# Performance work log

Measured on AMD Instinct MI355X. Metric: run time of the kernel, lower is better.

The kernel has to match this reference:

```python
import jax, jax.numpy as jnp
import numpy as np
from math import sqrt

N = 50000      # n_nodes
M = 800000     # n_edges (avg degree 16)
D = 256        # d_Embedding
H = 8          # heads
DK = 32        # per-head key/query dim
DV = 32        # per-head value dim


def setup_inputs() -> dict:
    key = jax.random.key(0)
    ks = jax.random.split(key, 10)
    s = 0.02
    x = jax.random.normal(ks[0], (N, D), dtype=jnp.float32)
    edge_index = jax.random.randint(ks[1], (2, M), 0, N, dtype=jnp.int32)
    # projection weights stored pre-reshaped to (D, H, dhead); equivalent to nn.Linear(D, H*dhead)
    Wk = jax.random.normal(ks[2], (D, H, DK), dtype=jnp.float32) * s
    bk = jax.random.normal(ks[3], (H, DK), dtype=jnp.float32) * s
    Wq = jax.random.normal(ks[4], (D, H, DK), dtype=jnp.float32) * s
    bq = jax.random.normal(ks[5], (H, DK), dtype=jnp.float32) * s
    Wv = jax.random.normal(ks[6], (D, H, DV), dtype=jnp.float32) * s
    bv = jax.random.normal(ks[7], (H, DV), dtype=jnp.float32) * s
    Wagg = jax.random.normal(ks[8], (H * DV, D), dtype=jnp.float32) * s
    bagg = jnp.zeros((D,), dtype=jnp.float32)
    Wff = jax.random.normal(ks[9], (D, D), dtype=jnp.float32) * s
    bff = jnp.zeros((D,), dtype=jnp.float32)
    return {"x": x, "edge_index": edge_index, "Wk": Wk, "bk": bk, "Wq": Wq,
            "bq": bq, "Wv": Wv, "bv": bv, "Wagg": Wagg, "bagg": bagg,
            "Wff": Wff, "bff": bff}


def reference(x, edge_index, Wk, bk, Wq, bq, Wv, bv, Wagg, bagg, Wff, bff):
    recv = edge_index[0]
    send = edge_index[1]
    # per-head projections: (N, H, d)
    K = jnp.einsum('nd,dhk->nhk', x, Wk) + bk
    Q = jnp.einsum('nd,dhk->nhk', x, Wq) + bq
    V = jnp.einsum('nd,dhv->nhv', x, Wv) + bv
    # edge-wise attention logits: (M, H)
    qk = jnp.sum(Q[recv] * K[send], axis=-1)
    # faithful to original: rescale by 3/global_max, then exp
    att = jnp.exp(qk * 3.0 / jnp.max(qk))
    # segment-softmax normalization over edges sharing a receiver
    sums = jax.ops.segment_sum(att, recv, num_segments=N)  # (N, H)
    att = att / sums[recv] / sqrt(DK)
    # weighted scatter-add of sender values: (N, H, DV)
    msg = att[..., None] * V[send]
    out = jax.ops.segment_sum(msg, recv, num_segments=N)
    out = jax.nn.relu(out).reshape(N, H * DV)
    out = jax.nn.relu(out @ Wagg + bagg)
    out = jax.nn.relu(out @ Wff + bff)
    return x + out
```

## Files before the change

kernel.cpp:

```cpp
#include <hip/hip_runtime.h>

#define N_NODES 50000
#define M_EDGES 800000
#define RP 50048

typedef __bf16 bf16x8 __attribute__((ext_vector_type(8)));
typedef __bf16 bf16x4 __attribute__((ext_vector_type(4)));
typedef float  f32x4  __attribute__((ext_vector_type(4)));

static __device__ __forceinline__ unsigned enc_ord(float f) {
    unsigned b = __float_as_uint(f);
    return (b & 0x80000000u) ? ~b : (b | 0x80000000u);
}
static __device__ __forceinline__ float dec_ord(unsigned u) {
    unsigned b = (u & 0x80000000u) ? (u ^ 0x80000000u) : ~u;
    return __uint_as_float(b);
}
static __device__ __forceinline__ float bflo(unsigned u) { return __uint_as_float(u << 16); }
static __device__ __forceinline__ float bfhi(unsigned u) { return __uint_as_float(u & 0xffff0000u); }
static __device__ __forceinline__ unsigned short bfbits(__bf16 b) {
    unsigned short u; __builtin_memcpy(&u, &b, 2); return u;
}

static __device__ __forceinline__ size_t PE(int m, int k) {
    return (size_t)(m >> 7) * 32768 + (size_t)(k >> 5) * 4096 +
           (size_t)((k >> 3) & 3) * 1024 + (size_t)(m & 127) * 8 + (k & 7);
}

static __device__ __forceinline__ void gload16(const void* g, void* l) {
    __builtin_amdgcn_global_load_lds(
        (const __attribute__((address_space(1))) void*)g,
        (__attribute__((address_space(3))) void*)l, 16, 0, 0);
}

static __device__ __forceinline__ void stage_panel(
    const char* a0, const char* a1, const char* b0, const char* b1,
    char* lds0, int buf, int t, int tid) {
    size_t so = (size_t)t * 8192 + (size_t)tid * 16;
    size_t lo = (size_t)buf * 32768 + (size_t)tid * 16;
    gload16(a0 + so, lds0 + lo);
    gload16(a0 + so + 4096, lds0 + lo + 4096);
    gload16(a1 + so, lds0 + 8192 + lo);
    gload16(a1 + so + 4096, lds0 + 8192 + lo + 4096);
    gload16(b0 + so, lds0 + 16384 + lo);
    gload16(b0 + so + 4096, lds0 + 16384 + lo + 4096);
    gload16(b1 + so, lds0 + 24576 + lo);
    gload16(b1 + so + 4096, lds0 + 24576 + lo + 4096);
}

__global__ __launch_bounds__(256) void prep_kernel(
    const float* __restrict__ Wk, const float* __restrict__ Wq,
    const float* __restrict__ Wv, const float* __restrict__ Wagg,
    const float* __restrict__ Wff,
    const float* __restrict__ bk, const float* __restrict__ bq,
    const float* __restrict__ bv,
    const float* __restrict__ X,
    __bf16* __restrict__ WHq, __bf16* __restrict__ WLq,
    __bf16* __restrict__ WaH, __bf16* __restrict__ WaL,
    __bf16* __restrict__ WfH, __bf16* __restrict__ WfL,
    float* __restrict__ bqkv, __bf16* __restrict__ xh, __bf16* __restrict__ xl,
    int* __restrict__ counts, int* __restrict__ cursor, unsigned* __restrict__ gmax) {
    int gid = blockIdx.x * 256 + threadIdx.x;
    int stride = gridDim.x * 256;
    for (int i = gid; i < 65536; i += stride) {
        int n = i >> 8, k = i & 255;
        size_t src = (size_t)k * 256 + n;
        float v; __bf16 h;
        v = Wk[src];   h = (__bf16)v; WHq[PE(n, k)] = h;
                       WLq[PE(n, k)] = (__bf16)(v - (float)h);
        v = Wq[src];   h = (__bf16)v; WHq[PE(n + 256, k)] = h;
                       WLq[PE(n + 256, k)] = (__bf16)(v - (float)h);
        v = Wv[src];   h = (__bf16)v; WHq[PE(n + 512, k)] = h;
                       WLq[PE(n + 512, k)] = (__bf16)(v - (float)h);
        v = Wagg[src]; h = (__bf16)v; WaH[PE(n, k)] = h;
                       WaL[PE(n, k)] = (__bf16)(v - (float)h);
        v = Wff[src];  h = (__bf16)v; WfH[PE(n, k)] = h;
                       WfL[PE(n, k)] = (__bf16)(v - (float)h);
    }
    const size_t nx = (size_t)N_NODES * 256 / 4;
    for (size_t i = gid; i < nx; i += stride) {
        float4 v = *(const float4*)(X + i * 4);
        int n = (int)(i >> 6), k0 = (int)((i * 4) & 255);
        bf16x4 hh, ll;
        hh[0] = (__bf16)v.x; ll[0] = (__bf16)(v.x - (float)hh[0]);
        hh[1] = (__bf16)v.y; ll[1] = (__bf16)(v.y - (float)hh[1]);
        hh[2] = (__bf16)v.z; ll[2] = (__bf16)(v.z - (float)hh[2]);
        hh[3] = (__bf16)v.w; ll[3] = (__bf16)(v.w - (float)hh[3]);
        size_t idx = PE(n, k0);
        *(bf16x4*)(xh + idx) = hh;
        *(bf16x4*)(xl + idx) = ll;
    }
    for (int i = gid; i < 768; i += stride)
        bqkv[i] = (i < 256) ? bk[i] : ((i < 512) ? bq[i - 256] : bv[i - 512]);
    for (int i = gid; i < N_NODES; i += stride) { counts[i] = 0; cursor[i] = 0; }
    if (gid == 0) *gmax = 0u;
}

__global__ __launch_bounds__(256) void gemm_qkv(
    const __bf16* __restrict__ AhP, const __bf16* __restrict__ AlP,
    const __bf16* __restrict__ BhP, const __bf16* __restrict__ BlP,
    const float* __restrict__ bqkv,
    __bf16* __restrict__ Kb, float* __restrict__ Qo, __bf16* __restrict__ Vb) {
    __shared__ __attribute__((aligned(16))) __bf16 sm[2][4][4][128][8];

    const int NB = 2346, q = NB / 8, r = NB % 8;
    int bid = blockIdx.x;
    int xcd = bid & 7, i0 = bid >> 3;
    int logical = (xcd < r ? xcd * (q + 1) : r * (q + 1) + (xcd - r) * q) + i0;
    int by = logical % 6;
    int bx = logical / 6;
    int row0 = bx * 128;
    int n0   = by * 128;

    int tid  = threadIdx.x;
    int lane = tid & 63, wave = tid >> 6;
    int wm = (wave >> 1) * 64, wn = (wave & 1) * 64;

    f32x4 acc[4][4];
    #pragma unroll
    for (int i = 0; i < 4; i++)
        #pragma unroll
        for (int j = 0; j < 4; j++) acc[i][j] = (f32x4)(0.f);

    const char* a0 = (const char*)AhP + (size_t)bx * 65536;
    const char* a1 = (const char*)AlP + (size_t)bx * 65536;
    const char* b0 = (const char*)BhP + (size_t)by * 65536;
    const char* b1 = (const char*)BlP + (size_t)by * 65536;
    char* lds0 = (char*)&sm[0][0][0][0][0];

    stage_panel(a0, a1, b0, b1, lds0, 0, 0, tid);
    __syncthreads();

    int h = lane >> 4;
    int m_base = wm + (lane & 15);
    int n_base = wn + (lane & 15);

    for (int t = 0; t < 8; t++) {
        int cur = t & 1;
        if (t < 7) stage_panel(a0, a1, b0, b1, lds0, cur ^ 1, t + 1, tid);
        bf16x8 ahf[4], alf[4], bhf[4], blf[4];
        #pragma unroll
        for (int mt = 0; mt < 4; mt++) {
            ahf[mt] = *(const bf16x8*)&sm[cur][0][h][m_base + mt * 16][0];
            alf[mt] = *(const bf16x8*)&sm[cur][1][h][m_base + mt * 16][0];
        }
        #pragma unroll
        for (int nt = 0; nt < 4; nt++) {
            bhf[nt] = *(const bf16x8*)&sm[cur][2][h][n_base + nt * 16][0];
            blf[nt] = *(const bf16x8*)&sm[cur][3][h][n_base + nt * 16][0];
        }
        #pragma unroll
        for (int mt = 0; mt < 4; mt++)
            #pragma unroll
            for (int nt = 0; nt < 4; nt++) {
                acc[mt][nt] = __builtin_amdgcn_mfma_f32_16x16x32_bf16(ahf[mt], bhf[nt], acc[mt][nt], 0, 0, 0);
                acc[mt][nt] = __builtin_amdgcn_mfma_f32_16x16x32_bf16(alf[mt], bhf[nt], acc[mt][nt], 0, 0, 0);
                acc[mt][nt] = __builtin_amdgcn_mfma_f32_16x16x32_bf16(ahf[mt], blf[nt], acc[mt][nt], 0, 0, 0);
            }
        __syncthreads();
    }

    #pragma unroll
    for (int mt = 0; mt < 4; mt++) {
        #pragma unroll
        for (int nt = 0; nt < 4; nt++) {
            int cg = n0 + wn + nt * 16 + (lane & 15);
            #pragma unroll
            for (int rr = 0; rr < 4; rr++) {
                int row = row0 + wm + mt * 16 + (lane >> 4) * 4 + rr;
                if (row < N_NODES) {
                    float v = acc[mt][nt][rr] + bqkv[cg];
                    if (cg < 256)      Kb[(size_t)row * 256 + cg] = (__bf16)v;
                    else if (cg < 512) Qo[(size_t)row * 256 + (cg - 256)] = v;
                    else               Vb[(size_t)row * 256 + (cg - 512)] = (__bf16)v;
                }
            }
        }
    }
}

__global__ void hist_kernel(const int* __restrict__ recv, int* __restrict__ counts) {
    int t = blockIdx.x * 256 + threadIdx.x;
    if (t < M_EDGES) atomicAdd(&counts[recv[t]], 1);
}

__global__ void scan_kernel(const int* __restrict__ counts, int* __restrict__ offsets) {
    __shared__ int part[256];
    int t = threadIdx.x;
    const int per = (N_NODES + 255) / 256;
    int start = t * per;
    int end = min(start + per, N_NODES);
    int s = 0;
    for (int i = start; i < end; i++) s += counts[i];
    part[t] = s;
    __syncthreads();
    if (t == 0) {
        int acc = 0;
        for (int i = 0; i < 256; i++) { int v = part[i]; part[i] = acc; acc += v; }
    }
    __syncthreads();
    int acc = part[t];
    for (int i = start; i < end; i++) { offsets[i] = acc; acc += counts[i]; }
    if (end == N_NODES && start < N_NODES) offsets[N_NODES] = acc;
}

__global__ void fill_kernel(const int* __restrict__ recv, const int* __restrict__ send,
                            const int* __restrict__ offsets,
                            int* __restrict__ cursor, int* __restrict__ ssorted,
                            int* __restrict__ rsorted) {
    int t = blockIdx.x * 256 + threadIdx.x;
    if (t < M_EDGES) {
        int r = recv[t];
        int pos = offsets[r] + atomicAdd(&cursor[r], 1);
        ssorted[pos] = send[t];
        rsorted[pos] = r;
    }
}

__global__ __launch_bounds__(256) void qk_csr_kernel(
    const int* __restrict__ ssorted, const int* __restrict__ rsorted,
    const float* __restrict__ Q, const unsigned short* __restrict__ Kb,
    float* __restrict__ qks, unsigned* __restrict__ gmax) {
    int wave_id = (blockIdx.x * 256 + threadIdx.x) >> 6;
    int lane = threadIdx.x & 63;
    int e_slot = lane >> 5;
    int sl = lane & 31;
    const int nwaves = (gridDim.x * 256) >> 6;
    const int npairs = M_EDGES / 2;
    float wmax = -INFINITY;
    for (int pp = wave_id; pp < npairs; pp += 4 * nwaves) {
        int ep[4]; bool valid[4];
        #pragma unroll
        for (int u = 0; u < 4; u++) {
            int p = pp + u * nwaves;
            valid[u] = p < npairs;
            ep[u] = (valid[u] ? p : pp) * 2 + e_slot;
        }
        int si[4], ri[4];
        #pragma unroll
        for (int u = 0; u < 4; u++) { si[u] = ssorted[ep[u]]; ri[u] = rsorted[ep[u]]; }
        uint4 kv[4]; float4 qa[4], qb[4];
        #pragma unroll
        for (int u = 0; u < 4; u++) {
            kv[u] = *(const uint4*)(Kb + (size_t)si[u] * 256 + sl * 8);
            qa[u] = *(const float4*)(Q + (size_t)ri[u] * 256 + sl * 8);
            qb[u] = *(const float4*)(Q + (size_t)ri[u] * 256 + sl * 8 + 4);
        }
        #pragma unroll
        for (int u = 0; u < 4; u++) {
            float d = qa[u].x * bflo(kv[u].x) + qa[u].y * bfhi(kv[u].x)
                    + qa[u].z * bflo(kv[u].y) + qa[u].w * bfhi(kv[u].y)
                    + qb[u].x * bflo(kv[u].z) + qb[u].y * bfhi(kv[u].z)
                    + qb[u].z * bflo(kv[u].w) + qb[u].w * bfhi(kv[u].w);
            d += __shfl_xor(d, 1);
            d += __shfl_xor(d, 2);
            wmax = fmaxf(wmax, d);
            if ((sl & 3) == 0 && valid[u])
                qks[(size_t)ep[u] * 8 + (sl >> 2)] = d;
        }
    }
    wmax = fmaxf(wmax, __shfl_xor(wmax, 1));
    wmax = fmaxf(wmax, __shfl_xor(wmax, 2));
    wmax = fmaxf(wmax, __shfl_xor(wmax, 4));
    wmax = fmaxf(wmax, __shfl_xor(wmax, 8));
    wmax = fmaxf(wmax, __shfl_xor(wmax, 16));
    wmax = fmaxf(wmax, __shfl_xor(wmax, 32));
    if (lane == 0 && wmax > -INFINITY) atomicMax(gmax, enc_ord(wmax));
}

__global__ __launch_bounds__(256) void node_agg_kernel(
    const int* __restrict__ offsets, const int* __restrict__ ssorted,
    const float* __restrict__ qks, const unsigned short* __restrict__ Vb,
    const unsigned* __restrict__ gmax,
    __bf16* __restrict__ msgH, __bf16* __restrict__ msgL) {
    int wave_id = (blockIdx.x * 256 + threadIdx.x) >> 6;
    int lane = threadIdx.x & 63;
    int h = lane >> 3;
    const int nwaves = (gridDim.x * 256) >> 6;
    const int per = (N_NODES + nwaves - 1) / nwaves;
    int n0 = wave_id * per;
    int nend = min(n0 + per, N_NODES);
    float scale = 3.0f / dec_ord(*gmax);
    for (int n = n0; n < nend; n++) {
        int off = offsets[n];
        int deg = offsets[n + 1] - off;
        float sum = 0.f, a0 = 0.f, a1 = 0.f, a2 = 0.f, a3 = 0.f;
        for (int b = 0; b < deg; b += 64) {
            int bn = min(64, deg - b);
            int idxb = ssorted[off + b + min(lane, bn - 1)];
            #define VROW(i) (*(const uint2*)(Vb + \
                (size_t)__shfl(idxb, min((i), bn - 1)) * 256 + lane * 4))
            #define QKL(i) qks[(size_t)(off + b + min((i), bn - 1)) * 8 + h]
            uint2 v0 = VROW(0);
            uint2 v1 = VROW(1);
            float q0 = QKL(0);
            float q1 = QKL(1);
            for (int i = 0; i < bn; i++) {
                uint2 vc = v0; v0 = v1; v1 = VROW(i + 2);
                float qc = q0; q0 = q1; q1 = QKL(i + 2);
                float a = __expf(qc * scale);
                sum += a;
                a0 += a * bflo(vc.x); a1 += a * bfhi(vc.x);
                a2 += a * bflo(vc.y); a3 += a * bfhi(vc.y);
            }
            #undef VROW
            #undef QKL
        }
        float inv = (deg > 0) ? 1.0f / (sum * 5.65685424949238f) : 0.f;
        float r0 = fmaxf(a0 * inv, 0.f), r1 = fmaxf(a1 * inv, 0.f);
        float r2 = fmaxf(a2 * inv, 0.f), r3 = fmaxf(a3 * inv, 0.f);
        bf16x4 hv, lv;
        hv[0] = (__bf16)r0; lv[0] = (__bf16)(r0 - (float)hv[0]);
        hv[1] = (__bf16)r1; lv[1] = (__bf16)(r1 - (float)hv[1]);
        hv[2] = (__bf16)r2; lv[2] = (__bf16)(r2 - (float)hv[2]);
        hv[3] = (__bf16)r3; lv[3] = (__bf16)(r3 - (float)hv[3]);
        size_t idx = PE(n, lane * 4);
        *(bf16x4*)(msgH + idx) = hv;
        *(bf16x4*)(msgL + idx) = lv;
    }
}

__global__ __launch_bounds__(256) void mlp_fused(
    const __bf16* __restrict__ msgHP, const __bf16* __restrict__ msgLP,
    const __bf16* __restrict__ WaHP, const __bf16* __restrict__ WaLP,
    const __bf16* __restrict__ WfHP, const __bf16* __restrict__ WfLP,
    const float* __restrict__ bagg, const float* __restrict__ bff,
    const float* __restrict__ x, float* __restrict__ out) {
    __shared__ __attribute__((aligned(16))) __bf16 sm[2][4][4][128][8];

    int row0 = blockIdx.x * 128;
    int bxp  = blockIdx.x;
    int tid  = threadIdx.x;
    int lane = tid & 63, wave = tid >> 6;
    int wm = (wave >> 1) * 64, wn = (wave & 1) * 64;
    char* lds0 = (char*)&sm[0][0][0][0][0];
    int h = lane >> 4;
    int m_base = wm + (lane & 15);
    int n_base = wn + (lane & 15);

    f32x4 acc1[2][4][4];
    #pragma unroll
    for (int nh = 0; nh < 2; nh++)
        #pragma unroll
        for (int i = 0; i < 4; i++)
            #pragma unroll
            for (int j = 0; j < 4; j++) acc1[nh][i][j] = (f32x4)(0.f);

    const char* a0 = (const char*)msgHP + (size_t)bxp * 65536;
    const char* a1 = (const char*)msgLP + (size_t)bxp * 65536;

    #pragma unroll
    for (int nh = 0; nh < 2; nh++) {
        const char* b0 = (const char*)WaHP + (size_t)nh * 65536;
        const char* b1 = (const char*)WaLP + (size_t)nh * 65536;
        stage_panel(a0, a1, b0, b1, lds0, 0, 0, tid);
        __syncthreads();
        for (int t = 0; t < 8; t++) {
            int cur = t & 1;
            if (t < 7) stage_panel(a0, a1, b0, b1, lds0, cur ^ 1, t + 1, tid);
            bf16x8 ahf[4], alf[4], bhf[4], blf[4];
            #pragma unroll
            for (int mt = 0; mt < 4; mt++) {
                ahf[mt] = *(const bf16x8*)&sm[cur][0][h][m_base + mt * 16][0];
                alf[mt] = *(const bf16x8*)&sm[cur][1][h][m_base + mt * 16][0];
            }
            #pragma unroll
            for (int nt = 0; nt < 4; nt++) {
                bhf[nt] = *(const bf16x8*)&sm[cur][2][h][n_base + nt * 16][0];
                blf[nt] = *(const bf16x8*)&sm[cur][3][h][n_base + nt * 16][0];
            }
            #pragma unroll
            for (int mt = 0; mt < 4; mt++)
                #pragma unroll
                for (int nt = 0; nt < 4; nt++) {
                    acc1[nh][mt][nt] = __builtin_amdgcn_mfma_f32_16x16x32_bf16(ahf[mt], bhf[nt], acc1[nh][mt][nt], 0, 0, 0);
                    acc1[nh][mt][nt] = __builtin_amdgcn_mfma_f32_16x16x32_bf16(alf[mt], bhf[nt], acc1[nh][mt][nt], 0, 0, 0);
                    acc1[nh][mt][nt] = __builtin_amdgcn_mfma_f32_16x16x32_bf16(ahf[mt], blf[nt], acc1[nh][mt][nt], 0, 0, 0);
                }
            __syncthreads();
        }
    }

    unsigned hidp[2][4][4][4];
    #pragma unroll
    for (int nh = 0; nh < 2; nh++)
        #pragma unroll
        for (int mt = 0; mt < 4; mt++)
            #pragma unroll
            for (int nt = 0; nt < 4; nt++)
                #pragma unroll
                for (int rr = 0; rr < 4; rr++) {
                    int col = nh * 128 + wn + nt * 16 + (lane & 15);
                    float v = acc1[nh][mt][nt][rr] + bagg[col];
                    v = fmaxf(v, 0.f);
                    __bf16 hh = (__bf16)v;
                    __bf16 hl = (__bf16)(v - (float)hh);
                    hidp[nh][mt][nt][rr] =
                        (unsigned)bfbits(hh) | ((unsigned)bfbits(hl) << 16);
                }

    unsigned short* chunkw = (unsigned short*)lds0;
    const __bf16*   chunkb = (const __bf16*)lds0;
    char*           b2c    = lds0 + 16384;
    const __bf16*   b2b    = (const __bf16*)(lds0 + 16384);

    for (int oh = 0; oh < 2; oh++) {
        const char* f0 = (const char*)WfHP + (size_t)oh * 65536;
        const char* f1 = (const char*)WfLP + (size_t)oh * 65536;
        f32x4 acc2[4][4];
        #pragma unroll
        for (int i = 0; i < 4; i++)
            #pragma unroll
            for (int j = 0; j < 4; j++) acc2[i][j] = (f32x4)(0.f);

        #pragma unroll
        for (int s = 0; s < 8; s++) {
            __syncthreads();
            int nh = s >> 2, sq = s & 3;
            if (wn == ((sq >= 2) ? 64 : 0)) {
                int nt0 = (sq & 1) * 2;
                #pragma unroll
                for (int mt = 0; mt < 4; mt++)
                    #pragma unroll
                    for (int j = 0; j < 2; j++) {
                        int nt = nt0 + j;
                        int kc = (wn + nt * 16 + (lane & 15)) - 32 * sq;
                        int ks = kc >> 3, e = kc & 7;
                        #pragma unroll
                        for (int rr = 0; rr < 4; rr++) {
                            int row = wm + mt * 16 + (lane >> 4) * 4 + rr;
                            unsigned u = hidp[nh][mt][nt][rr];
                            chunkw[(size_t)ks * 1024 + row * 8 + e] =
                                (unsigned short)(u & 0xffffu);
                            chunkw[(size_t)(4 + ks) * 1024 + row * 8 + e] =
                                (unsigned short)(u >> 16);
                        }
                    }
            }
            {
                size_t so = (size_t)s * 8192 + (size_t)tid * 16;
                size_t lo = (size_t)tid * 16;
                gload16(f0 + so, b2c + lo);
                gload16(f0 + so + 4096, b2c + lo + 4096);
                gload16(f1 + so, b2c + 8192 + lo);
                gload16(f1 + so + 4096, b2c + 8192 + lo + 4096);
            }
            __syncthreads();
            bf16x8 a2h[4], a2l[4], b2h[4], b2l[4];
            #pragma unroll
            for (int mt = 0; mt < 4; mt++) {
                a2h[mt] = *(const bf16x8*)&chunkb[(size_t)h * 1024 + (m_base + mt * 16) * 8];
                a2l[mt] = *(const bf16x8*)&chunkb[(size_t)(4 + h) * 1024 + (m_base + mt * 16) * 8];
            }
            #pragma unroll
            for (int nt = 0; nt < 4; nt++) {
                b2h[nt] = *(const bf16x8*)&b2b[(size_t)h * 1024 + (n_base + nt * 16) * 8];
                b2l[nt] = *(const bf16x8*)&b2b[(size_t)(4 + h) * 1024 + (n_base + nt * 16) * 8];
            }
            #pragma unroll
            for (int mt = 0; mt < 4; mt++)
                #pragma unroll
                for (int nt = 0; nt < 4; nt++) {
                    acc2[mt][nt] = __builtin_amdgcn_mfma_f32_16x16x32_bf16(a2h[mt], b2h[nt], acc2[mt][nt], 0, 0, 0);
                    acc2[mt][nt] = __builtin_amdgcn_mfma_f32_16x16x32_bf16(a2l[mt], b2h[nt], acc2[mt][nt], 0, 0, 0);
                    acc2[mt][nt] = __builtin_amdgcn_mfma_f32_16x16x32_bf16(a2h[mt], b2l[nt], acc2[mt][nt], 0, 0, 0);
                }
        }
        #pragma unroll
        for (int mt = 0; mt < 4; mt++)
            #pragma unroll
            for (int nt = 0; nt < 4; nt++) {
                int oc = oh * 128 + wn + nt * 16 + (lane & 15);
                #pragma unroll
                for (int rr = 0; rr < 4; rr++) {
                    int row = row0 + wm + mt * 16 + (lane >> 4) * 4 + rr;
                    if (row < N_NODES) {
                        float v = acc2[mt][nt][rr] + bff[oc];
                        v = fmaxf(v, 0.f);
                        size_t idx = (size_t)row * 256 + oc;
                        out[idx] = v + x[idx];
                    }
                }
            }
    }
}

extern "C" void kernel_launch(void* const* d_in, const int* in_sizes, int n_in,
                              void* d_out, int out_size, void* d_ws, size_t ws_size,
                              hipStream_t stream) {
    const float* x    = (const float*)d_in[0];
    const int*   edge = (const int*)d_in[1];
    const int*   recv = edge;
    const int*   send = edge + M_EDGES;
    const float* Wk   = (const float*)d_in[2];
    const float* bk   = (const float*)d_in[3];
    const float* Wq   = (const float*)d_in[4];
    const float* bq   = (const float*)d_in[5];
    const float* Wv   = (const float*)d_in[6];
    const float* bv   = (const float*)d_in[7];
    const float* Wagg = (const float*)d_in[8];
    const float* bagg = (const float*)d_in[9];
    const float* Wff  = (const float*)d_in[10];
    const float* bff  = (const float*)d_in[11];
    float* out = (float*)d_out;

    float*  Qbuf  = (float*)d_ws;
    float*  reg2  = Qbuf + (size_t)RP * 256;
    float*  qks   = reg2 + (size_t)RP * 256;
    __bf16* Kbf   = (__bf16*)(qks + (size_t)M_EDGES * 8);
    __bf16* Vbf   = Kbf + (size_t)RP * 256;
    int* counts   = (int*)(Vbf + (size_t)RP * 256);
    int* cursor   = counts + N_NODES;
    int* offsets  = cursor + N_NODES;
    int* ssorted  = offsets + N_NODES + 1;
    unsigned* gmax = (unsigned*)(ssorted + M_EDGES);
    __bf16* wt    = (__bf16*)(gmax + 1);
    __bf16* WHq = wt;
    __bf16* WLq = wt + 3 * 65536;
    __bf16* WaH = wt + 6 * 65536;  __bf16* WaL = wt + 7 * 65536;
    __bf16* WfH = wt + 8 * 65536;  __bf16* WfL = wt + 9 * 65536;
    float* bqkv = (float*)(wt + 10 * 65536);
    __bf16* xh   = (__bf16*)reg2;
    __bf16* xl   = xh + (size_t)RP * 256;
    int*    rsorted = (int*)reg2;
    __bf16* msgH = (__bf16*)reg2;
    __bf16* msgL = msgH + (size_t)RP * 256;

    dim3 blk(256);
    dim3 edge_grid((M_EDGES + 255) / 256);

    hipLaunchKernelGGL(prep_kernel, dim3(2048), blk, 0, stream,
                       Wk, Wq, Wv, Wagg, Wff, bk, bq, bv, x,
                       WHq, WLq, WaH, WaL, WfH, WfL, bqkv, xh, xl,
                       counts, cursor, gmax);
    hipLaunchKernelGGL(gemm_qkv, dim3(2346), blk, 0, stream,
                       xh, xl, WHq, WLq, bqkv, Kbf, Qbuf, Vbf);
    hipLaunchKernelGGL(hist_kernel, edge_grid, blk, 0, stream, recv, counts);
    hipLaunchKernelGGL(scan_kernel, dim3(1), blk, 0, stream, counts, offsets);
    hipLaunchKernelGGL(fill_kernel, edge_grid, blk, 0, stream, recv, send, offsets,
                       cursor, ssorted, rsorted);
    hipLaunchKernelGGL(qk_csr_kernel, dim3(1024), blk, 0, stream,
                       ssorted, rsorted, Qbuf, (const unsigned short*)Kbf, qks, gmax);
    hipLaunchKernelGGL(node_agg_kernel, dim3(2048), blk, 0, stream,
                       offsets, ssorted, qks, (const unsigned short*)Vbf, gmax,
                       msgH, msgL);
    hipLaunchKernelGGL(mlp_fused, dim3((N_NODES + 127) / 128), blk, 0, stream,
                       msgH, msgL, WaH, WaL, WfH, WfL, bagg, bff, x, out);
}
```

Measured before the change: 834.1 us.

## Stage activations in LDS once and read weight fragments directly from global memory

The fused MLP kernel now loads each block's message tile into LDS in two halves, used across both output halves, instead of re-staging activations alongside weights per panel. Wagg and Wff fragments are read straight from global memory, which should hit L2 or cache since all blocks share them, so LDS weight staging and many barriers go away. The second GEMM writes all four hidden sub-chunks per K-half before computing, which cuts synchronization count. The cost is global-load latency on the MFMA critical path without double buffering, and higher register pressure from the full unroll.

New measurement: 825.5 us. About the same (-1.0%).

```diff
diff --git a/kernel.cpp b/kernel.cpp
--- a/kernel.cpp
+++ b/kernel.cpp
@@ -326,18 +326,20 @@
     const __bf16* __restrict__ WfHP, const __bf16* __restrict__ WfLP,
     const float* __restrict__ bagg, const float* __restrict__ bff,
     const float* __restrict__ x, float* __restrict__ out) {
-    __shared__ __attribute__((aligned(16))) __bf16 sm[2][4][4][128][8];
+    __shared__ __attribute__((aligned(16))) __bf16 sm[32768];
 
     int row0 = blockIdx.x * 128;
-    int bxp  = blockIdx.x;
     int tid  = threadIdx.x;
     int lane = tid & 63, wave = tid >> 6;
     int wm = (wave >> 1) * 64, wn = (wave & 1) * 64;
-    char* lds0 = (char*)&sm[0][0][0][0][0];
+    char* lds0 = (char*)sm;
     int h = lane >> 4;
     int m_base = wm + (lane & 15);
     int n_base = wn + (lane & 15);
 
+    const char* a0 = (const char*)msgHP + (size_t)blockIdx.x * 65536;
+    const char* a1 = (const char*)msgLP + (size_t)blockIdx.x * 65536;
+
     f32x4 acc1[2][4][4];
     #pragma unroll
     for (int nh = 0; nh < 2; nh++)
@@ -346,37 +348,60 @@
             #pragma unroll
             for (int j = 0; j < 4; j++) acc1[nh][i][j] = (f32x4)(0.f);
 
-    const char* a0 = (const char*)msgHP + (size_t)bxp * 65536;
-    const char* a1 = (const char*)msgLP + (size_t)bxp * 65536;
-
-    #pragma unroll
-    for (int nh = 0; nh < 2; nh++) {
-        const char* b0 = (const char*)WaHP + (size_t)nh * 65536;
-        const char* b1 = (const char*)WaLP + (size_t)nh * 65536;
-        stage_panel(a0, a1, b0, b1, lds0, 0, 0, tid);
-        __syncthreads();
-        for (int t = 0; t < 8; t++) {
-            int cur = t & 1;
-            if (t < 7) stage_panel(a0, a1, b0, b1, lds0, cur ^ 1, t + 1, tid);
-            bf16x8 ahf[4], alf[4], bhf[4], blf[4];
-            #pragma unroll
-            for (int mt = 0; mt < 4; mt++) {
-                ahf[mt] = *(const bf16x8*)&sm[cur][0][h][m_base + mt * 16][0];
-                alf[mt] = *(const bf16x8*)&sm[cur][1][h][m_base + mt * 16][0];
-            }
-            #pragma unroll
-            for (int nt = 0; nt < 4; nt++) {
-                bhf[nt] = *(const bf16x8*)&sm[cur][2][h][n_base + nt * 16][0];
-                blf[nt] = *(const bf16x8*)&sm[cur][3][h][n_base + nt * 16][0];
-            }
-            #pragma unroll
-            for (int mt = 0; mt < 4; mt++)
+    #pragma unroll
+    for (int tl = 0; tl < 4; tl++) {
+        size_t so = (size_t)tl * 8192 + (size_t)tid * 16;
+        gload16(a0 + so, lds0 + so);
+        gload16(a0 + so + 4096, lds0 + so + 4096);
+        gload16(a1 + so, lds0 + 32768 + so);
+        gload16(a1 + so + 4096, lds0 + 32768 + so + 4096);
+    }
+    __syncthreads();
+
+    #pragma unroll
+    for (int hf = 0; hf < 2; hf++) {
+        #pragma unroll
+        for (int nh = 0; nh < 2; nh++) {
+            const __bf16* wb0 = WaHP + (size_t)nh * 32768;
+            const __bf16* wb1 = WaLP + (size_t)nh * 32768;
+            #pragma unroll
+            for (int tl = 0; tl < 4; tl++) {
+                int t = hf * 4 + tl;
+                const __bf16* lA = (const __bf16*)lds0;
+                bf16x8 ahf[4], alf[4], bhf[4], blf[4];
+                #pragma unroll
+                for (int mt = 0; mt < 4; mt++) {
+                    size_t ai = (size_t)tl * 4096 + (size_t)h * 1024 + (size_t)(m_base + mt * 16) * 8;
+                    ahf[mt] = *(const bf16x8*)&lA[ai];
+                    alf[mt] = *(const bf16x8*)&lA[16384 + ai];
+                }
                 #pragma unroll
                 for (int nt = 0; nt < 4; nt++) {
-                    acc1[nh][mt][nt] = __builtin_amdgcn_mfma_f32_16x16x32_bf16(ahf[mt], bhf[nt], acc1[nh][mt][nt], 0, 0, 0);
-                    acc1[nh][mt][nt] = __builtin_amdgcn_mfma_f32_16x16x32_bf16(alf[mt], bhf[nt], acc1[nh][mt][nt], 0, 0, 0);
-                    acc1[nh][mt][nt] = __builtin_amdgcn_mfma_f32_16x16x32_bf16(ahf[mt], blf[nt], acc1[nh][mt][nt], 0, 0, 0);
-                }
+                    size_t bi = (size_t)t * 4096 + (size_t)h * 1024 + (size_t)(n_base + nt * 16) * 8;
+                    bhf[nt] = *(const bf16x8*)(wb0 + bi);
+                    blf[nt] = *(const bf16x8*)(wb1 + bi);
+                }
+                #pragma unroll
+                for (int mt = 0; mt < 4; mt++)
+                    #pragma unroll
+                    for (int nt = 0; nt < 4; nt++) {
+                        acc1[nh][mt][nt] = __builtin_amdgcn_mfma_f32_16x16x32_bf16(ahf[mt], bhf[nt], acc1[nh][mt][nt], 0, 0, 0);
+                        acc1[nh][mt][nt] = __builtin_amdgcn_mfma_f32_16x16x32_bf16(alf[mt], bhf[nt], acc1[nh][mt][nt], 0, 0, 0);
+                        acc1[nh][mt][nt] = __builtin_amdgcn_mfma_f32_16x16x32_bf16(ahf[mt], blf[nt], acc1[nh][mt][nt], 0, 0, 0);
+                    }
+            }
+        }
+        if (hf == 0) {
+            __syncthreads();
+            #pragma unroll
+            for (int tl = 0; tl < 4; tl++) {
+                size_t so = (size_t)(4 + tl) * 8192 + (size_t)tid * 16;
+                size_t lo = (size_t)tl * 8192 + (size_t)tid * 16;
+                gload16(a0 + so, lds0 + lo);
+                gload16(a0 + so + 4096, lds0 + lo + 4096);
+                gload16(a1 + so, lds0 + 32768 + lo);
+                gload16(a1 + so + 4096, lds0 + 32768 + lo + 4096);
+            }
             __syncthreads();
         }
     }
@@ -399,14 +424,13 @@
                         (unsigned)bfbits(hh) | ((unsigned)bfbits(hl) << 16);
                 }
 
-    unsigned short* chunkw = (unsigned short*)lds0;
-    const __bf16*   chunkb = (const __bf16*)lds0;
-    char*           b2c    = lds0 + 16384;
-    const __bf16*   b2b    = (const __bf16*)(lds0 + 16384);
-
+    unsigned short* w16 = (unsigned short*)lds0;
+    const __bf16*   lB  = (const __bf16*)lds0;
+
+    #pragma unroll
     for (int oh = 0; oh < 2; oh++) {
-        const char* f0 = (const char*)WfHP + (size_t)oh * 65536;
-        const char* f1 = (const char*)WfLP + (size_t)oh * 65536;
+        const __bf16* f0 = WfHP + (size_t)oh * 32768;
+        const __bf16* f1 = WfLP + (size_t)oh * 32768;
         f32x4 acc2[4][4];
         #pragma unroll
         for (int i = 0; i < 4; i++)
@@ -414,57 +438,57 @@
             for (int j = 0; j < 4; j++) acc2[i][j] = (f32x4)(0.f);
 
         #pragma unroll
-        for (int s = 0; s < 8; s++) {
+        for (int kh = 0; kh < 2; kh++) {
             __syncthreads();
-            int nh = s >> 2, sq = s & 3;
-            if (wn == ((sq >= 2) ? 64 : 0)) {
-                int nt0 = (sq & 1) * 2;
+            #pragma unroll
+            for (int sl = 0; sl < 4; sl++) {
+                if (wn == ((sl >= 2) ? 64 : 0)) {
+                    int nt0 = (sl & 1) * 2;
+                    #pragma unroll
+                    for (int mt = 0; mt < 4; mt++)
+                        #pragma unroll
+                        for (int j = 0; j < 2; j++) {
+                            int nt = nt0 + j;
+                            int kc = (wn + nt * 16 + (lane & 15)) - 32 * sl;
+                            int ks = kc >> 3, e = kc & 7;
+                            #pragma unroll
+                            for (int rr = 0; rr < 4; rr++) {
+                                int row = wm + mt * 16 + (lane >> 4) * 4 + rr;
+                                unsigned u = hidp[kh][mt][nt][rr];
+                                w16[(size_t)sl * 4096 + ks * 1024 + row * 8 + e] =
+                                    (unsigned short)(u & 0xffffu);
+                                w16[16384 + (size_t)sl * 4096 + ks * 1024 + row * 8 + e] =
+                                    (unsigned short)(u >> 16);
+                            }
+                        }
+                }
+            }
+            __syncthreads();
+            #pragma unroll
+            for (int tl = 0; tl < 4; tl++) {
+                int t = kh * 4 + tl;
+                bf16x8 a2h[4], a2l[4], b2h[4], b2l[4];
+                #pragma unroll
+                for (int mt = 0; mt < 4; mt++) {
+                    size_t ai = (size_t)tl * 4096 + (size_t)h * 1024 + (size_t)(m_base + mt * 16) * 8;
+                    a2h[mt] = *(const bf16x8*)&lB[ai];
+                    a2l[mt] = *(const bf16x8*)&lB[16384 + ai];
+                }
+                #pragma unroll
+                for (int nt = 0; nt < 4; nt++) {
+                    size_t bi = (size_t)t * 4096 + (size_t)h * 1024 + (size_t)(n_base + nt * 16) * 8;
+                    b2h[nt] = *(const bf16x8*)(f0 + bi);
+                    b2l[nt] = *(const bf16x8*)(f1 + bi);
+                }
                 #pragma unroll
                 for (int mt = 0; mt < 4; mt++)
                     #pragma unroll
-                    for (int j = 0; j < 2; j++) {
-                        int nt = nt0 + j;
-                        int kc = (wn + nt * 16 + (lane & 15)) - 32 * sq;
-                        int ks = kc >> 3, e = kc & 7;
-                        #pragma unroll
-                        for (int rr = 0; rr < 4; rr++) {
-                            int row = wm + mt * 16 + (lane >> 4) * 4 + rr;
-                            unsigned u = hidp[nh][mt][nt][rr];
-                            chunkw[(size_t)ks * 1024 + row * 8 + e] =
-                                (unsigned short)(u & 0xffffu);
-                            chunkw[(size_t)(4 + ks) * 1024 + row * 8 + e] =
-                                (unsigned short)(u >> 16);
-                        }
+                    for (int nt = 0; nt < 4; nt++) {
+                        acc2[mt][nt] = __builtin_amdgcn_mfma_f32_16x16x32_bf16(a2h[mt], b2h[nt], acc2[mt][nt], 0, 0, 0);
+                        acc2[mt][nt] = __builtin_amdgcn_mfma_f32_16x16x32_bf16(a2l[mt], b2h[nt], acc2[mt][nt], 0, 0, 0);
+                        acc2[mt][nt] = __builtin_amdgcn_mfma_f32_16x16x32_bf16(a2h[mt], b2l[nt], acc2[mt][nt], 0, 0, 0);
                     }
             }
-            {
-                size_t so = (size_t)s * 8192 + (size_t)tid * 16;
-                size_t lo = (size_t)tid * 16;
-                gload16(f0 + so, b2c + lo);
-                gload16(f0 + so + 4096, b2c + lo + 4096);
-                gload16(f1 + so, b2c + 8192 + lo);
-                gload16(f1 + so + 4096, b2c + 8192 + lo + 4096);
-            }
-            __syncthreads();
-            bf16x8 a2h[4], a2l[4], b2h[4], b2l[4];
-            #pragma unroll
-            for (int mt = 0; mt < 4; mt++) {
-                a2h[mt] = *(const bf16x8*)&chunkb[(size_t)h * 1024 + (m_base + mt * 16) * 8];
-                a2l[mt] = *(const bf16x8*)&chunkb[(size_t)(4 + h) * 1024 + (m_base + mt * 16) * 8];
-            }
-            #pragma unroll
-            for (int nt = 0; nt < 4; nt++) {
-                b2h[nt] = *(const bf16x8*)&b2b[(size_t)h * 1024 + (n_base + nt * 16) * 8];
-                b2l[nt] = *(const bf16x8*)&b2b[(size_t)(4 + h) * 1024 + (n_base + nt * 16) * 8];
-            }
-            #pragma unroll
-            for (int mt = 0; mt < 4; mt++)
-                #pragma unroll
-                for (int nt = 0; nt < 4; nt++) {
-                    acc2[mt][nt] = __builtin_amdgcn_mfma_f32_16x16x32_bf16(a2h[mt], b2h[nt], acc2[mt][nt], 0, 0, 0);
-                    acc2[mt][nt] = __builtin_amdgcn_mfma_f32_16x16x32_bf16(a2l[mt], b2h[nt], acc2[mt][nt], 0, 0, 0);
-                    acc2[mt][nt] = __builtin_amdgcn_mfma_f32_16x16x32_bf16(a2h[mt], b2l[nt], acc2[mt][nt], 0, 0, 0);
-                }
         }
         #pragma unroll
         for (int mt = 0; mt < 4; mt++)
```

## Restructure fused MLP to 64-row tiles with weights read directly from global

Applied to the files above, without the earlier changes.

The fused two-layer MLP kernel now processes 64 rows per block instead of 128, doubling the grid. Each wave owns 64 output columns across all rows. Only the activation panel is staged in shared memory, while the weight fragments for both GEMMs are loaded straight from global memory (and so from cache) instead of being staged through LDS. The aim is to cut LDS use and synchronisation, raise occupancy, and keep the hidden layer in-block with fewer exchanges. The cost is repeated global weight reads per wave and less A-tile reuse per block.

Measured after the change: 769.5 us. 1.08x faster.

```diff
diff --git a/kernel.cpp b/kernel.cpp
--- a/kernel.cpp
+++ b/kernel.cpp
@@ -326,136 +326,142 @@
     const __bf16* __restrict__ WfHP, const __bf16* __restrict__ WfLP,
     const float* __restrict__ bagg, const float* __restrict__ bff,
     const float* __restrict__ x, float* __restrict__ out) {
-    __shared__ __attribute__((aligned(16))) __bf16 sm[2][4][4][128][8];
-
-    int row0 = blockIdx.x * 128;
-    int bxp  = blockIdx.x;
+    __shared__ __attribute__((aligned(16))) __bf16 sm[16384];
+
+    int row0 = blockIdx.x * 64;
+    int p    = blockIdx.x >> 1;
+    int sb   = blockIdx.x & 1;
     int tid  = threadIdx.x;
     int lane = tid & 63, wave = tid >> 6;
-    int wm = (wave >> 1) * 64, wn = (wave & 1) * 64;
-    char* lds0 = (char*)&sm[0][0][0][0][0];
-    int h = lane >> 4;
-    int m_base = wm + (lane & 15);
-    int n_base = wn + (lane & 15);
-
-    f32x4 acc1[2][4][4];
-    #pragma unroll
-    for (int nh = 0; nh < 2; nh++)
-        #pragma unroll
-        for (int i = 0; i < 4; i++)
-            #pragma unroll
-            for (int j = 0; j < 4; j++) acc1[nh][i][j] = (f32x4)(0.f);
-
-    const char* a0 = (const char*)msgHP + (size_t)bxp * 65536;
-    const char* a1 = (const char*)msgLP + (size_t)bxp * 65536;
-
-    #pragma unroll
-    for (int nh = 0; nh < 2; nh++) {
-        const char* b0 = (const char*)WaHP + (size_t)nh * 65536;
-        const char* b1 = (const char*)WaLP + (size_t)nh * 65536;
-        stage_panel(a0, a1, b0, b1, lds0, 0, 0, tid);
-        __syncthreads();
-        for (int t = 0; t < 8; t++) {
-            int cur = t & 1;
-            if (t < 7) stage_panel(a0, a1, b0, b1, lds0, cur ^ 1, t + 1, tid);
+    int wn   = wave * 64;
+    int h    = lane >> 4;
+    int ml   = lane & 15;
+    char* lds0 = (char*)sm;
+    const __bf16* lA = (const __bf16*)sm;
+
+    const char* a0 = (const char*)msgHP + (size_t)p * 65536;
+    const char* a1 = (const char*)msgLP + (size_t)p * 65536;
+
+#define STAGE_A(hf) do {                                                      \
+        _Pragma("unroll")                                                     \
+        for (int tl = 0; tl < 4; tl++) {                                      \
+            size_t so = (size_t)((hf) * 4 + tl) * 8192 +                      \
+                        (size_t)(tid >> 6) * 2048 + (size_t)sb * 1024 +       \
+                        (size_t)(tid & 63) * 16;                              \
+            size_t lo = (size_t)tl * 4096 + (size_t)tid * 16;                 \
+            gload16(a0 + so, lds0 + lo);                                      \
+            gload16(a1 + so, lds0 + 16384 + lo);                              \
+        }                                                                     \
+    } while (0)
+
+    f32x4 acc1[4][4];
+    #pragma unroll
+    for (int i = 0; i < 4; i++)
+        #pragma unroll
+        for (int j = 0; j < 4; j++) acc1[i][j] = (f32x4)(0.f);
+
+    STAGE_A(0);
+    __syncthreads();
+
+    #pragma unroll
+    for (int hf = 0; hf < 2; hf++) {
+        #pragma unroll
+        for (int tl = 0; tl < 4; tl++) {
+            int t = hf * 4 + tl;
             bf16x8 ahf[4], alf[4], bhf[4], blf[4];
             #pragma unroll
             for (int mt = 0; mt < 4; mt++) {
-                ahf[mt] = *(const bf16x8*)&sm[cur][0][h][m_base + mt * 16][0];
-                alf[mt] = *(const bf16x8*)&sm[cur][1][h][m_base + mt * 16][0];
+                size_t ai = (size_t)tl * 2048 + (size_t)h * 512 + (size_t)(ml + mt * 16) * 8;
+                ahf[mt] = *(const bf16x8*)&lA[ai];
+                alf[mt] = *(const bf16x8*)&lA[8192 + ai];
             }
             #pragma unroll
             for (int nt = 0; nt < 4; nt++) {
-                bhf[nt] = *(const bf16x8*)&sm[cur][2][h][n_base + nt * 16][0];
-                blf[nt] = *(const bf16x8*)&sm[cur][3][h][n_base + nt * 16][0];
+                int c = wn + nt * 16 + ml;
+                size_t bi = (size_t)(c >> 7) * 32768 + (size_t)t * 4096 +
+                            (size_t)h * 1024 + (size_t)(c & 127) * 8;
+                bhf[nt] = *(const bf16x8*)(WaHP + bi);
+                blf[nt] = *(const bf16x8*)(WaLP + bi);
             }
             #pragma unroll
             for (int mt = 0; mt < 4; mt++)
                 #pragma unroll
                 for (int nt = 0; nt < 4; nt++) {
-                    acc1[nh][mt][nt] = __builtin_amdgcn_mfma_f32_16x16x32_bf16(ahf[mt], bhf[nt], acc1[nh][mt][nt], 0, 0, 0);
-                    acc1[nh][mt][nt] = __builtin_amdgcn_mfma_f32_16x16x32_bf16(alf[mt], bhf[nt], acc1[nh][mt][nt], 0, 0, 0);
-                    acc1[nh][mt][nt] = __builtin_amdgcn_mfma_f32_16x16x32_bf16(ahf[mt], blf[nt], acc1[nh][mt][nt], 0, 0, 0);
+                    acc1[mt][nt] = __builtin_amdgcn_mfma_f32_16x16x32_bf16(ahf[mt], bhf[nt], acc1[mt][nt], 0, 0, 0);
+                    acc1[mt][nt] = __builtin_amdgcn_mfma_f32_16x16x32_bf16(alf[mt], bhf[nt], acc1[mt][nt], 0, 0, 0);
+                    acc1[mt][nt] = __builtin_amdgcn_mfma_f32_16x16x32_bf16(ahf[mt], blf[nt], acc1[mt][nt], 0, 0, 0);
                 }
+        }
+        if (hf == 0) {
             __syncthreads();
-        }
-    }
-
-    unsigned hidp[2][4][4][4];
-    #pragma unroll
-    for (int nh = 0; nh < 2; nh++)
-        #pragma unroll
-        for (int mt = 0; mt < 4; mt++)
-            #pragma unroll
-            for (int nt = 0; nt < 4; nt++)
-                #pragma unroll
-                for (int rr = 0; rr < 4; rr++) {
-                    int col = nh * 128 + wn + nt * 16 + (lane & 15);
-                    float v = acc1[nh][mt][nt][rr] + bagg[col];
-                    v = fmaxf(v, 0.f);
-                    __bf16 hh = (__bf16)v;
-                    __bf16 hl = (__bf16)(v - (float)hh);
-                    hidp[nh][mt][nt][rr] =
-                        (unsigned)bfbits(hh) | ((unsigned)bfbits(hl) << 16);
-                }
-
-    unsigned short* chunkw = (unsigned short*)lds0;
-    const __bf16*   chunkb = (const __bf16*)lds0;
-    char*           b2c    = lds0 + 16384;
-    const __bf16*   b2b    = (const __bf16*)(lds0 + 16384);
-
-    for (int oh = 0; oh < 2; oh++) {
-        const char* f0 = (const char*)WfHP + (size_t)oh * 65536;
-        const char* f1 = (const char*)WfLP + (size_t)oh * 65536;
-        f32x4 acc2[4][4];
-        #pragma unroll
-        for (int i = 0; i < 4; i++)
-            #pragma unroll
-            for (int j = 0; j < 4; j++) acc2[i][j] = (f32x4)(0.f);
-
-        #pragma unroll
-        for (int s = 0; s < 8; s++) {
+            STAGE_A(1);
             __syncthreads();
-            int nh = s >> 2, sq = s & 3;
-            if (wn == ((sq >= 2) ? 64 : 0)) {
-                int nt0 = (sq & 1) * 2;
+        }
+    }
+#undef STAGE_A
+
+    unsigned hidp[4][4][4];
+    #pragma unroll
+    for (int mt = 0; mt < 4; mt++)
+        #pragma unroll
+        for (int nt = 0; nt < 4; nt++)
+            #pragma unroll
+            for (int rr = 0; rr < 4; rr++) {
+                int col = wn + nt * 16 + ml;
+                float v = acc1[mt][nt][rr] + bagg[col];
+                v = fmaxf(v, 0.f);
+                __bf16 hh = (__bf16)v;
+                __bf16 hl = (__bf16)(v - (float)hh);
+                hidp[mt][nt][rr] = (unsigned)bfbits(hh) | ((unsigned)bfbits(hl) << 16);
+            }
+
+    unsigned short* w16 = (unsigned short*)sm;
+    f32x4 acc2[4][4];
+    #pragma unroll
+    for (int i = 0; i < 4; i++)
+        #pragma unroll
+        for (int j = 0; j < 4; j++) acc2[i][j] = (f32x4)(0.f);
+
+    #pragma unroll
+    for (int kh = 0; kh < 2; kh++) {
+        __syncthreads();
+        if ((wave >> 1) == kh) {
+            int base = (wave & 1) * 64;
+            #pragma unroll
+            for (int nt = 0; nt < 4; nt++) {
+                int lk = base + nt * 16 + ml;
+                int tl = lk >> 5, ks = (lk >> 3) & 3, e = lk & 7;
                 #pragma unroll
                 for (int mt = 0; mt < 4; mt++)
                     #pragma unroll
-                    for (int j = 0; j < 2; j++) {
-                        int nt = nt0 + j;
-                        int kc = (wn + nt * 16 + (lane & 15)) - 32 * sq;
-                        int ks = kc >> 3, e = kc & 7;
-                        #pragma unroll
-                        for (int rr = 0; rr < 4; rr++) {
-                            int row = wm + mt * 16 + (lane >> 4) * 4 + rr;
-                            unsigned u = hidp[nh][mt][nt][rr];
-                            chunkw[(size_t)ks * 1024 + row * 8 + e] =
-                                (unsigned short)(u & 0xffffu);
-                            chunkw[(size_t)(4 + ks) * 1024 + row * 8 + e] =
-                                (unsigned short)(u >> 16);
-                        }
+                    for (int rr = 0; rr < 4; rr++) {
+                        int row = mt * 16 + (lane >> 4) * 4 + rr;
+                        size_t di = (size_t)tl * 2048 + (size_t)ks * 512 +
+                                    (size_t)row * 8 + e;
+                        unsigned u = hidp[mt][nt][rr];
+                        w16[di] = (unsigned short)(u & 0xffffu);
+                        w16[8192 + di] = (unsigned short)(u >> 16);
                     }
             }
-            {
-                size_t so = (size_t)s * 8192 + (size_t)tid * 16;
-                size_t lo = (size_t)tid * 16;
-                gload16(f0 + so, b2c + lo);
-                gload16(f0 + so + 4096, b2c + lo + 4096);
-                gload16(f1 + so, b2c + 8192 + lo);
-                gload16(f1 + so + 4096, b2c + 8192 + lo + 4096);
-            }
-            __syncthreads();
+        }
+        __syncthreads();
+        #pragma unroll
+        for (int tl = 0; tl < 4; tl++) {
+            int t = kh * 4 + tl;
             bf16x8 a2h[4], a2l[4], b2h[4], b2l[4];
             #pragma unroll
             for (int mt = 0; mt < 4; mt++) {
-                a2h[mt] = *(const bf16x8*)&chunkb[(size_t)h * 1024 + (m_base + mt * 16) * 8];
-                a2l[mt] = *(const bf16x8*)&chunkb[(size_t)(4 + h) * 1024 + (m_base + mt * 16) * 8];
+                size_t ai = (size_t)tl * 2048 + (size_t)h * 512 + (size_t)(ml + mt * 16) * 8;
+                a2h[mt] = *(const bf16x8*)&lA[ai];
+                a2l[mt] = *(const bf16x8*)&lA[8192 + ai];
             }
             #pragma unroll
             for (int nt = 0; nt < 4; nt++) {
-                b2h[nt] = *(const bf16x8*)&b2b[(size_t)h * 1024 + (n_base + nt * 16) * 8];
-                b2l[nt] = *(const bf16x8*)&b2b[(size_t)(4 + h) * 1024 + (n_base + nt * 16) * 8];
+                int oc = wn + nt * 16 + ml;
+                size_t bi = (size_t)(oc >> 7) * 32768 + (size_t)t * 4096 +
+                            (size_t)h * 1024 + (size_t)(oc & 127) * 8;
+                b2h[nt] = *(const bf16x8*)(WfHP + bi);
+                b2l[nt] = *(const bf16x8*)(WfLP + bi);
             }
             #pragma unroll
             for (int mt = 0; mt < 4; mt++)
@@ -466,23 +472,23 @@
                     acc2[mt][nt] = __builtin_amdgcn_mfma_f32_16x16x32_bf16(a2h[mt], b2l[nt], acc2[mt][nt], 0, 0, 0);
                 }
         }
-        #pragma unroll
-        for (int mt = 0; mt < 4; mt++)
-            #pragma unroll
-            for (int nt = 0; nt < 4; nt++) {
-                int oc = oh * 128 + wn + nt * 16 + (lane & 15);
-                #pragma unroll
-                for (int rr = 0; rr < 4; rr++) {
-                    int row = row0 + wm + mt * 16 + (lane >> 4) * 4 + rr;
-                    if (row < N_NODES) {
-                        float v = acc2[mt][nt][rr] + bff[oc];
-                        v = fmaxf(v, 0.f);
-                        size_t idx = (size_t)row * 256 + oc;
-                        out[idx] = v + x[idx];
-                    }
+    }
+    #pragma unroll
+    for (int mt = 0; mt < 4; mt++)
+        #pragma unroll
+        for (int nt = 0; nt < 4; nt++) {
+            int oc = wn + nt * 16 + ml;
+            #pragma unroll
+            for (int rr = 0; rr < 4; rr++) {
+                int row = row0 + mt * 16 + (lane >> 4) * 4 + rr;
+                if (row < N_NODES) {
+                    float v = acc2[mt][nt][rr] + bff[oc];
+                    v = fmaxf(v, 0.f);
+                    size_t idx = (size_t)row * 256 + oc;
+                    out[idx] = v + x[idx];
                 }
             }
-    }
+        }
 }
 
 extern "C" void kernel_launch(void* const* d_in, const int* in_sizes, int n_in,
@@ -544,6 +550,6 @@
     hipLaunchKernelGGL(node_agg_kernel, dim3(2048), blk, 0, stream,
                        offsets, ssorted, qks, (const unsigned short*)Vbf, gmax,
                        msgH, msgL);
-    hipLaunchKernelGGL(mlp_fused, dim3((N_NODES + 127) / 128), blk, 0, stream,
+    hipLaunchKernelGGL(mlp_fused, dim3((N_NODES + 63) / 64), blk, 0, stream,
                        msgH, msgL, WaH, WaL, WfH, WfL, bagg, bff, x, out);
 }
```
